# Kernel tuning notes

Hardware: AMD Instinct MI355X
Metric: run time of the kernel (lower is better)

The kernel has to match this reference:

```python
import jax, jax.numpy as jnp
import numpy as np

N, E, B, D, R, L = 60000, 600000, 512, 128, 30, 3
CUT_LOW, CUT_HIGH = 0.0, 10.0
N_ATOM_TYPES = 100


def _sp(x, beta, threshold):
    # torch.nn.Softplus(beta, threshold): x if beta*x > threshold else log1p(exp(beta*x))/beta
    bx = beta * x
    return jnp.where(bx > threshold, x, jnp.log1p(jnp.exp(jnp.minimum(bx, threshold))) / beta)


def setup_inputs() -> dict:
    key = jax.random.key(0)
    ks = jax.random.split(key, 16)

    def lin(k, fi, fo):
        k1, k2 = jax.random.split(k)
        W = jax.random.normal(k1, (fi, fo), jnp.float32) * (fi ** -0.5)
        b = jax.random.normal(k2, (fo,), jnp.float32) * 0.01
        return W, b

    def lin_stack(k, fi, fo, n):
        Ws, bs = zip(*[lin(kk, fi, fo) for kk in jax.random.split(k, n)])
        return jnp.stack(Ws), jnp.stack(bs)

    inp = {}
    inp['atom_type'] = jax.random.randint(ks[0], (N,), 0, N_ATOM_TYPES)
    inp['src'] = jax.random.randint(ks[1], (E,), 0, N)
    inp['dst'] = jax.random.randint(ks[2], (E,), 0, N)
    inp['graph_ids'] = jnp.sort(jax.random.randint(ks[3], (N,), 0, B))
    inp['dist'] = jax.random.uniform(ks[4], (E,), jnp.float32) * CUT_HIGH
    inp['node_emb'] = jax.random.normal(ks[5], (N_ATOM_TYPES, D), jnp.float32) * 0.1
    inp['W_n1'], inp['b_n1'] = lin_stack(ks[6], D, D, L)
    inp['W_c1'], inp['b_c1'] = lin_stack(ks[7], R, D, L)
    inp['W_c2'], inp['b_c2'] = lin_stack(ks[8], D, D, L)
    inp['W_c3'], inp['b_c3'] = lin_stack(ks[9], D, D, L)
    inp['W_n2'], inp['b_n2'] = lin_stack(ks[10], D, D, L)
    inp['W_n3'], inp['b_n3'] = lin_stack(ks[11], D, D, L)
    inp['W_r1'], inp['b_r1'] = lin(ks[12], D * (L + 1), 64)
    inp['W_r2'], inp['b_r2'] = lin(ks[13], 64, 1)
    return inp


def reference(atom_type, src, dst, graph_ids, dist, node_emb,
              W_n1, b_n1, W_c1, b_c1, W_c2, b_c2, W_c3, b_c3,
              W_n2, b_n2, W_n3, b_n3, W_r1, b_r1, W_r2, b_r2):
    # RBF expansion of edge distances: exp(-(d - mu_k)^2 / gap)  -> [E, R]
    centers = jnp.linspace(CUT_LOW, CUT_HIGH, R).astype(dist.dtype)
    gap = centers[1] - centers[0]
    rbf = jnp.exp(-((dist[:, None] - centers) ** 2) / gap)

    h = node_emb[atom_type]  # node embedding lookup [N, D]
    hs = [h]
    for i in range(L):  # MultiLevelInteraction layers (fixed small count)
        h_new = hs[-1] @ W_n1[i] + b_n1[i]                       # node_layer1 [N, D]
        # VEConv edge MLP on rbf (linear1 -> softplus(0.5,14) -> linear2 -> linear3)
        e = _sp(rbf @ W_c1[i] + b_c1[i], 0.5, 14.0) @ W_c2[i] + b_c2[i]
        e = e @ W_c3[i] + b_c3[i]                                 # [E, D]
        # sum_e(h_new[src]*e) + sum_e(e) fused into one scatter-sum over dst
        msg = (h_new[src] + 1.0) * e                              # [E, D]
        node = jax.ops.segment_sum(msg, dst, num_segments=N)      # [N, D]
        new_node = _sp(node @ W_n2[i] + b_n2[i], 0.5, 14.0) @ W_n3[i] + b_n3[i]
        hs.append(hs[-1] + new_node)                              # residual h_i
    hcat = jnp.concatenate(hs, axis=1)                            # [N, D*(L+1)]
    out = _sp(hcat @ W_r1 + b_r1, 1.0, 20.0) @ W_r2 + b_r2        # [N, 1]
    # dgl.sum_nodes per molecule, then flatten -> [B]
    return jax.ops.segment_sum(out[:, 0], graph_ids, num_segments=B)
```

## Files before the change

kernel.cpp:

```cpp
#include <hip/hip_runtime.h>
#include <math.h>

#define N_NODES 60000
#define N_EDGES 600000
#define B_GRAPHS 512
#define DIM 128
#define RBF_R 30
#define NLAYERS 3
#define NBINS 1024
#define CHUNK 512
#define NCHUNK ((N_NODES + CHUNK - 1) / CHUNK)

typedef __attribute__((ext_vector_type(8))) short bf16x8;
typedef __attribute__((ext_vector_type(4))) float f32x4;

__device__ __forceinline__ float sp05(float x) {
    float bx = 0.5f * x;
    return bx > 14.0f ? x : 2.0f * log1pf(expf(bx));
}
__device__ __forceinline__ float sp1(float x) {
    return x > 20.0f ? x : log1pf(expf(x));
}
__device__ __forceinline__ unsigned short f2bf(float f) {
    unsigned int u = __float_as_uint(f);
    unsigned int r = u + 0x7FFFu + ((u >> 16) & 1u);
    return (unsigned short)(r >> 16);
}
__device__ __forceinline__ float bf2f(unsigned int s) {
    return __uint_as_float(s << 16);
}


__global__ void k_convW(const float* __restrict__ Wn1, const float* __restrict__ Wn2,
                        const float* __restrict__ Wn3, unsigned short* __restrict__ WtF) {
    int i = blockIdx.x * 256 + threadIdx.x;
    int mat = i >> 14, r = i & 16383;
    int frag = r >> 9, within = r & 511;
    int ks = frag >> 3, ntile = frag & 7;
    int lane = within >> 3, j = within & 7;
    int q = lane >> 4, l16 = lane & 15;
    int n = ntile * 16 + l16;
    int k = ks * 32 + q * 8 + j;
    const float* src = (mat < 3) ? (Wn1 + (size_t)mat * 16384)
                     : (mat < 6) ? (Wn2 + (size_t)(mat - 3) * 16384)
                                 : (Wn3 + (size_t)(mat - 6) * 16384);
    WtF[i] = f2bf(src[k * 128 + n]);
}

__global__ void k_convR(const float* __restrict__ Wr1, unsigned short* __restrict__ Wr1tF) {
    int i = blockIdx.x * 256 + threadIdx.x;
    int frag = i >> 9, within = i & 511;
    int lvl = frag >> 4, ks = (frag >> 2) & 3, ntile = frag & 3;
    int lane = within >> 3, j = within & 7;
    int q = lane >> 4, l16 = lane & 15;
    int n = ntile * 16 + l16;
    int k = lvl * 128 + ks * 32 + q * 8 + j;
    Wr1tF[i] = f2bf(Wr1[k * 64 + n]);
}

__global__ void k_embed(const int* __restrict__ atom_type,
                        const float* __restrict__ node_emb,
                        float* __restrict__ h0, unsigned short* __restrict__ hb0) {
    int i = blockIdx.x * blockDim.x + threadIdx.x;
    if (i >= N_NODES * DIM) return;
    int n = i >> 7, d = i & 127;
    float v = node_emb[atom_type[n] * DIM + d];
    h0[i] = v;
    hb0[i] = f2bf(v);
}


__global__ void k_hist(const int* __restrict__ dst, int* __restrict__ counts) {
    int e = blockIdx.x * blockDim.x + threadIdx.x;
    if (e >= N_EDGES) return;
    atomicAdd(&counts[dst[e]], 1);
}

__global__ void k_bsum(const int* __restrict__ counts, int* __restrict__ bsums) {
    __shared__ int red[256];
    int c = blockIdx.x, tid = threadIdx.x;
    int base = c * CHUNK;
    int v = 0;
    for (int i = tid; i < CHUNK; i += 256)
        if (base + i < N_NODES) v += counts[base + i];
    red[tid] = v;
    __syncthreads();
    for (int s = 128; s > 0; s >>= 1) {
        if (tid < s) red[tid] += red[tid + s];
        __syncthreads();
    }
    if (tid == 0) bsums[c] = red[0];
}

__global__ void k_scan_b(int* __restrict__ bsums) {
    __shared__ int sb[NCHUNK];
    int tid = threadIdx.x;
    if (tid < NCHUNK) sb[tid] = bsums[tid];
    __syncthreads();
    if (tid == 0) {
        int run = 0;
        for (int i = 0; i < NCHUNK; ++i) { int v = sb[i]; sb[i] = run; run += v; }
    }
    __syncthreads();
    if (tid < NCHUNK) bsums[tid] = sb[tid];
}

__global__ void k_scan_final(const int* __restrict__ counts, const int* __restrict__ bsums,
                             int* __restrict__ offsets) {
    __shared__ int sc[CHUNK];
    int c = blockIdx.x, tid = threadIdx.x;
    int base = c * CHUNK;
    for (int i = tid; i < CHUNK; i += 256)
        sc[i] = (base + i < N_NODES) ? counts[base + i] : 0;
    __syncthreads();
    if (tid == 0) {
        int run = bsums[c];
        for (int i = 0; i < CHUNK; ++i) { int v = sc[i]; sc[i] = run; run += v; }
    }
    __syncthreads();
    for (int i = tid; i < CHUNK; i += 256)
        if (base + i < N_NODES) offsets[base + i] = sc[i];
    if (c == 0 && tid == 0) offsets[N_NODES] = N_EDGES;
}

__global__ void k_fill(const int* __restrict__ src, const int* __restrict__ dst,
                       const float* __restrict__ dist,
                       const int* __restrict__ offsets, int* __restrict__ cnt2,
                       int* __restrict__ srcp, int* __restrict__ binp,
                       float* __restrict__ wp) {
    int e = blockIdx.x * blockDim.x + threadIdx.x;
    if (e >= N_EDGES) return;
    int d = dst[e];
    int pos = offsets[d] + atomicAdd(&cnt2[d], 1);
    srcp[pos] = src[e];
    float x = dist[e];
    float p = x * ((float)NBINS / 10.0f);
    int bin = (int)p;
    if (bin > NBINS - 1) bin = NBINS - 1;
    binp[pos] = bin;
    wp[pos] = p - (float)bin;
}


__global__ void k_table(const float* __restrict__ Wc1, const float* __restrict__ bc1,
                        const float* __restrict__ Wc2, const float* __restrict__ bc2,
                        const float* __restrict__ Wc3, const float* __restrict__ bc3,
                        unsigned short* __restrict__ tableb) {
    __shared__ float t[DIM];
    __shared__ float u[DIM];
    int b = blockIdx.x;
    int d = threadIdx.x;
    float dist = (float)b * (10.0f / (float)NBINS);
    const float gap = 10.0f / 29.0f;
    float acc = bc1[d];
#pragma unroll
    for (int k = 0; k < RBF_R; ++k) {
        float c = (float)k * (10.0f / 29.0f);
        float df = dist - c;
        acc += expf(-df * df / gap) * Wc1[k * DIM + d];
    }
    t[d] = sp05(acc);
    __syncthreads();
    acc = bc2[d];
#pragma unroll 8
    for (int k = 0; k < DIM; ++k) acc += t[k] * Wc2[k * DIM + d];
    u[d] = acc;
    __syncthreads();
    acc = bc3[d];
#pragma unroll 8
    for (int k = 0; k < DIM; ++k) acc += u[k] * Wc3[k * DIM + d];
    tableb[b * DIM + d] = f2bf(acc);
}

__global__ void k_pack(const unsigned short* __restrict__ tableb,
                       unsigned int* __restrict__ packed) {
    int i = blockIdx.x * 256 + threadIdx.x;
    float a = bf2f(tableb[i]);
    float b = bf2f(tableb[i + DIM]);
    packed[i] = (unsigned int)f2bf(a) | ((unsigned int)f2bf(b - a) << 16);
}

__global__ __launch_bounds__(256) void k_gemm_g(const unsigned short* __restrict__ Ab,
                                                const unsigned short* __restrict__ WtF,
                                                const float* __restrict__ bias,
                                                unsigned short* __restrict__ Cb) {
    int tid = threadIdx.x;
    int wave = tid >> 6, lane = tid & 63;
    int q = lane >> 4, l16 = lane & 15;
    int mhalf = wave & 1, nhalf = wave >> 1;
    int rb = blockIdx.x * 64 + mhalf * 32;
    int c0 = nhalf * 64;
    bf16x8 bfrag[4][4];
#pragma unroll
    for (int ks = 0; ks < 4; ++ks)
#pragma unroll
        for (int nt = 0; nt < 4; ++nt)
            bfrag[ks][nt] = *(const bf16x8*)&WtF[(size_t)(ks * 8 + nhalf * 4 + nt) * 512 + lane * 8];
    f32x4 acc[2][4] = {};
#pragma unroll
    for (int ks = 0; ks < 4; ++ks)
#pragma unroll
        for (int mt = 0; mt < 2; ++mt) {
            int m = rb + mt * 16 + l16;
            if (m > N_NODES - 1) m = N_NODES - 1;
            bf16x8 a = *(const bf16x8*)&Ab[(size_t)m * 128 + ks * 32 + q * 8];
#pragma unroll
            for (int nt = 0; nt < 4; ++nt)
                acc[mt][nt] = __builtin_amdgcn_mfma_f32_16x16x32_bf16(a, bfrag[ks][nt], acc[mt][nt], 0, 0, 0);
        }
#pragma unroll
    for (int mt = 0; mt < 2; ++mt)
#pragma unroll
        for (int nt = 0; nt < 4; ++nt) {
            int col = c0 + nt * 16 + l16;
            float b = bias[col] + 1.0f;
#pragma unroll
            for (int r = 0; r < 4; ++r) {
                int row = rb + mt * 16 + q * 4 + r;
                if (row < N_NODES) Cb[(size_t)row * 128 + col] = f2bf(acc[mt][nt][r] + b);
            }
        }
}

__global__ __launch_bounds__(256) void k_gather(
    const int* __restrict__ offsets, const int* __restrict__ srcp,
    const int* __restrict__ binp, const float* __restrict__ wp,
    const unsigned int* __restrict__ packed, const unsigned short* __restrict__ gb,
    unsigned short* __restrict__ nodeb) {
    int wave = threadIdx.x >> 6, lane = threadIdx.x & 63;
    int n = blockIdx.x * 4 + wave;
    int beg = offsets[n], end = offsets[n + 1];
    float acc0 = 0.f, acc1 = 0.f, acc2 = 0.f, acc3 = 0.f;
    int j = beg;
    for (; j + 2 <= end; j += 2) {
        int s0 = srcp[j],   s1 = srcp[j + 1];
        int b0 = binp[j],   b1 = binp[j + 1];
        float w0 = wp[j],   w1 = wp[j + 1];
        uint2 p0 = *(const uint2*)&packed[(size_t)b0 * DIM + lane * 2];
        uint2 p1 = *(const uint2*)&packed[(size_t)b1 * DIM + lane * 2];
        unsigned int g0 = *(const unsigned int*)&gb[(size_t)s0 * DIM + lane * 2];
        unsigned int g1 = *(const unsigned int*)&gb[(size_t)s1 * DIM + lane * 2];
        acc0 += bf2f(g0 & 0xffff) * (bf2f(p0.x & 0xffff) + w0 * bf2f(p0.x >> 16));
        acc1 += bf2f(g0 >> 16)    * (bf2f(p0.y & 0xffff) + w0 * bf2f(p0.y >> 16));
        acc2 += bf2f(g1 & 0xffff) * (bf2f(p1.x & 0xffff) + w1 * bf2f(p1.x >> 16));
        acc3 += bf2f(g1 >> 16)    * (bf2f(p1.y & 0xffff) + w1 * bf2f(p1.y >> 16));
    }
    if (j < end) {
        int s0 = srcp[j];
        int b0 = binp[j];
        float w0 = wp[j];
        uint2 p0 = *(const uint2*)&packed[(size_t)b0 * DIM + lane * 2];
        unsigned int g0 = *(const unsigned int*)&gb[(size_t)s0 * DIM + lane * 2];
        acc0 += bf2f(g0 & 0xffff) * (bf2f(p0.x & 0xffff) + w0 * bf2f(p0.x >> 16));
        acc1 += bf2f(g0 >> 16)    * (bf2f(p0.y & 0xffff) + w0 * bf2f(p0.y >> 16));
    }
    acc0 += acc2; acc1 += acc3;
    unsigned int o = (unsigned int)f2bf(acc0) | ((unsigned int)f2bf(acc1) << 16);
    *(unsigned int*)&nodeb[(size_t)n * DIM + lane * 2] = o;
}

__global__ __launch_bounds__(256) void k_node_update(
    const unsigned short* __restrict__ nodeb,
    const unsigned short* __restrict__ W2tF, const float* __restrict__ b2,
    const unsigned short* __restrict__ W3tF, const float* __restrict__ b3,
    const float* __restrict__ h_in, float* __restrict__ h_out,
    unsigned short* __restrict__ hb_out) {
    __shared__ unsigned short ts[64][136];
    int tid = threadIdx.x;
    int wave = tid >> 6, lane = tid & 63;
    int q = lane >> 4, l16 = lane & 15;
    int mhalf = wave & 1, nhalf = wave >> 1;
    int rb = blockIdx.x * 64 + mhalf * 32;
    int c0 = nhalf * 64;

    bf16x8 bfrag[4][4];
#pragma unroll
    for (int ks = 0; ks < 4; ++ks)
#pragma unroll
        for (int nt = 0; nt < 4; ++nt)
            bfrag[ks][nt] = *(const bf16x8*)&W2tF[(size_t)(ks * 8 + nhalf * 4 + nt) * 512 + lane * 8];
    f32x4 acc[2][4] = {};
#pragma unroll
    for (int ks = 0; ks < 4; ++ks)
#pragma unroll
        for (int mt = 0; mt < 2; ++mt) {
            int m = rb + mt * 16 + l16;
            if (m > N_NODES - 1) m = N_NODES - 1;
            bf16x8 a = *(const bf16x8*)&nodeb[(size_t)m * 128 + ks * 32 + q * 8];
#pragma unroll
            for (int nt = 0; nt < 4; ++nt)
                acc[mt][nt] = __builtin_amdgcn_mfma_f32_16x16x32_bf16(a, bfrag[ks][nt], acc[mt][nt], 0, 0, 0);
        }
#pragma unroll
    for (int mt = 0; mt < 2; ++mt)
#pragma unroll
        for (int nt = 0; nt < 4; ++nt) {
            int col = c0 + nt * 16 + l16;
            float b = b2[col];
#pragma unroll
            for (int r = 0; r < 4; ++r) {
                int lrow = mhalf * 32 + mt * 16 + q * 4 + r;
                ts[lrow][col] = f2bf(sp05(acc[mt][nt][r] + b));
            }
        }
    __syncthreads();
#pragma unroll
    for (int ks = 0; ks < 4; ++ks)
#pragma unroll
        for (int nt = 0; nt < 4; ++nt)
            bfrag[ks][nt] = *(const bf16x8*)&W3tF[(size_t)(ks * 8 + nhalf * 4 + nt) * 512 + lane * 8];
#pragma unroll
    for (int mt = 0; mt < 2; ++mt)
#pragma unroll
        for (int nt = 0; nt < 4; ++nt) acc[mt][nt] = (f32x4){0.f, 0.f, 0.f, 0.f};
#pragma unroll
    for (int ks = 0; ks < 4; ++ks)
#pragma unroll
        for (int mt = 0; mt < 2; ++mt) {
            int lrow = mhalf * 32 + mt * 16 + l16;
            bf16x8 a = *(const bf16x8*)&ts[lrow][ks * 32 + q * 8];
#pragma unroll
            for (int nt = 0; nt < 4; ++nt)
                acc[mt][nt] = __builtin_amdgcn_mfma_f32_16x16x32_bf16(a, bfrag[ks][nt], acc[mt][nt], 0, 0, 0);
        }
#pragma unroll
    for (int mt = 0; mt < 2; ++mt)
#pragma unroll
        for (int nt = 0; nt < 4; ++nt) {
            int col = c0 + nt * 16 + l16;
            float b = b3[col];
#pragma unroll
            for (int r = 0; r < 4; ++r) {
                int row = rb + mt * 16 + q * 4 + r;
                if (row < N_NODES) {
                    size_t idx = (size_t)row * 128 + col;
                    float v = h_in[idx] + acc[mt][nt][r] + b;
                    h_out[idx] = v;
                    hb_out[idx] = f2bf(v);
                }
            }
        }
}

__global__ __launch_bounds__(256) void k_readout(
    const unsigned short* __restrict__ hb0, const unsigned short* __restrict__ hb1,
    const unsigned short* __restrict__ hb2, const unsigned short* __restrict__ hb3,
    const unsigned short* __restrict__ Wr1tF, const float* __restrict__ br1,
    const float* __restrict__ Wr2, const float* __restrict__ br2,
    const int* __restrict__ graph_ids, float* __restrict__ out) {
    int tid = threadIdx.x;
    int wave = tid >> 6, lane = tid & 63;
    int q = lane >> 4, l16 = lane & 15;
    int rb = blockIdx.x * 64 + wave * 16;
    const unsigned short* hbs[4] = {hb0, hb1, hb2, hb3};
    f32x4 acc[4] = {};
    for (int lvl = 0; lvl < 4; ++lvl) {
        bf16x8 bfrag[4][4];
#pragma unroll
        for (int ks = 0; ks < 4; ++ks)
#pragma unroll
            for (int nt = 0; nt < 4; ++nt)
                bfrag[ks][nt] = *(const bf16x8*)&Wr1tF[(size_t)((lvl * 4 + ks) * 4 + nt) * 512 + lane * 8];
        const unsigned short* Ab = hbs[lvl];
#pragma unroll
        for (int ks = 0; ks < 4; ++ks) {
            int m = rb + l16;
            if (m > N_NODES - 1) m = N_NODES - 1;
            bf16x8 a = *(const bf16x8*)&Ab[(size_t)m * 128 + ks * 32 + q * 8];
#pragma unroll
            for (int nt = 0; nt < 4; ++nt)
                acc[nt] = __builtin_amdgcn_mfma_f32_16x16x32_bf16(a, bfrag[ks][nt], acc[nt], 0, 0, 0);
        }
    }
    float brr = br2[0];
    float partial[4] = {0.f, 0.f, 0.f, 0.f};
#pragma unroll
    for (int nt = 0; nt < 4; ++nt) {
        int col = nt * 16 + l16;
        float b = br1[col];
        float w = Wr2[col];
#pragma unroll
        for (int r = 0; r < 4; ++r) partial[r] += sp1(acc[nt][r] + b) * w;
    }
#pragma unroll
    for (int r = 0; r < 4; ++r) {
        float v = partial[r];
        v += __shfl_xor(v, 1); v += __shfl_xor(v, 2);
        v += __shfl_xor(v, 4); v += __shfl_xor(v, 8);
        if (l16 == 0) {
            int row = rb + q * 4 + r;
            if (row < N_NODES) atomicAdd(&out[graph_ids[row]], v + brr);
        }
    }
}

extern "C" void kernel_launch(void* const* d_in, const int* in_sizes, int n_in,
                              void* d_out, int out_size, void* d_ws, size_t ws_size,
                              hipStream_t stream) {
    const int* atom_type   = (const int*)d_in[0];
    const int* src         = (const int*)d_in[1];
    const int* dst         = (const int*)d_in[2];
    const int* graph_ids   = (const int*)d_in[3];
    const float* dist      = (const float*)d_in[4];
    const float* node_emb  = (const float*)d_in[5];
    const float* W_n1 = (const float*)d_in[6];  const float* b_n1 = (const float*)d_in[7];
    const float* W_c1 = (const float*)d_in[8];  const float* b_c1 = (const float*)d_in[9];
    const float* W_c2 = (const float*)d_in[10]; const float* b_c2 = (const float*)d_in[11];
    const float* W_c3 = (const float*)d_in[12]; const float* b_c3 = (const float*)d_in[13];
    const float* W_n2 = (const float*)d_in[14]; const float* b_n2 = (const float*)d_in[15];
    const float* W_n3 = (const float*)d_in[16]; const float* b_n3 = (const float*)d_in[17];
    const float* W_r1 = (const float*)d_in[18]; const float* b_r1 = (const float*)d_in[19];
    const float* W_r2 = (const float*)d_in[20]; const float* b_r2 = (const float*)d_in[21];
    float* out = (float*)d_out;

    size_t ND = (size_t)N_NODES * DIM;
    float* h_even = (float*)d_ws;
    float* h_odd  = h_even + ND;
    float* wp     = h_odd + ND;
    int* offsets  = (int*)(wp + N_EDGES);
    int* srcp     = offsets + 60008;
    int* binp     = srcp + N_EDGES;
    int* counts   = binp + N_EDGES;
    int* cnt2     = counts + N_NODES;
    int* bsums    = cnt2 + N_NODES;
    unsigned int* packed = (unsigned int*)(bsums + 128);
    unsigned short* hb0    = (unsigned short*)(packed + (size_t)NBINS * DIM);
    unsigned short* hb1    = hb0 + ND;
    unsigned short* hb2    = hb1 + ND;
    unsigned short* hb3    = hb2 + ND;
    unsigned short* gb     = hb3 + ND;
    unsigned short* nodeb  = gb + ND;
    unsigned short* tableb = nodeb + ND;
    unsigned short* WtF    = tableb + (size_t)(NBINS + 1) * DIM;
    unsigned short* Wr1tF  = WtF + 9 * 16384;

    unsigned short* hbp[4] = {hb0, hb1, hb2, hb3};
    float* hcur = h_even;
    float* hnext = h_odd;

    hipMemsetAsync(out, 0, B_GRAPHS * sizeof(float), stream);
    hipMemsetAsync(counts, 0, (2 * N_NODES + 128) * sizeof(int), stream);

    k_convW<<<(9 * 16384) / 256, 256, 0, stream>>>(W_n1, W_n2, W_n3, WtF);
    k_convR<<<32768 / 256, 256, 0, stream>>>(W_r1, Wr1tF);
    k_embed<<<(N_NODES * DIM) / 256, 256, 0, stream>>>(atom_type, node_emb, h_even, hb0);

    k_hist<<<(N_EDGES + 255) / 256, 256, 0, stream>>>(dst, counts);
    k_bsum<<<NCHUNK, 256, 0, stream>>>(counts, bsums);
    k_scan_b<<<1, 128, 0, stream>>>(bsums);
    k_scan_final<<<NCHUNK, 256, 0, stream>>>(counts, bsums, offsets);
    k_fill<<<(N_EDGES + 255) / 256, 256, 0, stream>>>(src, dst, dist, offsets, cnt2,
                                                      srcp, binp, wp);

    int gblocks = (N_NODES + 63) / 64;
    for (int i = 0; i < NLAYERS; ++i) {
        k_table<<<NBINS + 1, DIM, 0, stream>>>(
            W_c1 + (size_t)i * RBF_R * DIM, b_c1 + (size_t)i * DIM,
            W_c2 + (size_t)i * DIM * DIM,  b_c2 + (size_t)i * DIM,
            W_c3 + (size_t)i * DIM * DIM,  b_c3 + (size_t)i * DIM, tableb);
        k_pack<<<(NBINS * DIM) / 256, 256, 0, stream>>>(tableb, packed);
        k_gemm_g<<<gblocks, 256, 0, stream>>>(
            hbp[i], WtF + (size_t)i * 16384, b_n1 + (size_t)i * DIM, gb);
        k_gather<<<N_NODES / 4, 256, 0, stream>>>(offsets, srcp, binp, wp, packed, gb, nodeb);
        k_node_update<<<gblocks, 256, 0, stream>>>(
            nodeb, WtF + (size_t)(3 + i) * 16384, b_n2 + (size_t)i * DIM,
            WtF + (size_t)(6 + i) * 16384, b_n3 + (size_t)i * DIM,
            hcur, hnext, hbp[i + 1]);
        float* tmp = hcur; hcur = hnext; hnext = tmp;
    }
    k_readout<<<gblocks, 256, 0, stream>>>(
        hb0, hb1, hb2, hb3, Wr1tF, b_r1, W_r2, b_r2, graph_ids, out);
}
```

Baseline: 669.8 us.

## Pack edge metadata into uint2, unroll gather by four, restructure readout tiling

Edge source, bin index and quantized interpolation weight are packed into one 8-byte record per edge, so the gather kernel does one load instead of three separate array loads. The gather loop is unrolled to four edges per iteration to keep more independent memory requests in flight. The readout kernel stages the full W_r1 fragment set in shared memory and processes 128 rows per block with two M tiles, reusing the B fragments across both. The interpolation weight is now quantized to 16 bits, which adds a small precision loss, and the readout uses 64KB of LDS per block, which may reduce occupancy.

```diff
diff --git a/kernel.cpp b/kernel.cpp
--- a/kernel.cpp
+++ b/kernel.cpp
@@ -126,19 +126,19 @@
 __global__ void k_fill(const int* __restrict__ src, const int* __restrict__ dst,
                        const float* __restrict__ dist,
                        const int* __restrict__ offsets, int* __restrict__ cnt2,
-                       int* __restrict__ srcp, int* __restrict__ binp,
-                       float* __restrict__ wp) {
+                       uint2* __restrict__ meta) {
     int e = blockIdx.x * blockDim.x + threadIdx.x;
     if (e >= N_EDGES) return;
     int d = dst[e];
     int pos = offsets[d] + atomicAdd(&cnt2[d], 1);
-    srcp[pos] = src[e];
     float x = dist[e];
     float p = x * ((float)NBINS / 10.0f);
     int bin = (int)p;
     if (bin > NBINS - 1) bin = NBINS - 1;
-    binp[pos] = bin;
-    wp[pos] = p - (float)bin;
+    float w = p - (float)bin;
+    int wq = (int)(w * 65535.0f + 0.5f);
+    if (wq > 65535) wq = 65535;
+    meta[pos] = make_uint2((unsigned)src[e], ((unsigned)bin << 16) | (unsigned)wq);
 }
 
 
@@ -223,40 +223,50 @@
 }
 
 __global__ __launch_bounds__(256) void k_gather(
-    const int* __restrict__ offsets, const int* __restrict__ srcp,
-    const int* __restrict__ binp, const float* __restrict__ wp,
+    const int* __restrict__ offsets, const uint2* __restrict__ meta,
     const unsigned int* __restrict__ packed, const unsigned short* __restrict__ gb,
     unsigned short* __restrict__ nodeb) {
     int wave = threadIdx.x >> 6, lane = threadIdx.x & 63;
     int n = blockIdx.x * 4 + wave;
     int beg = offsets[n], end = offsets[n + 1];
+    int off = lane * 2;
+    const float ws = 1.0f / 65535.0f;
     float acc0 = 0.f, acc1 = 0.f, acc2 = 0.f, acc3 = 0.f;
     int j = beg;
-    for (; j + 2 <= end; j += 2) {
-        int s0 = srcp[j],   s1 = srcp[j + 1];
-        int b0 = binp[j],   b1 = binp[j + 1];
-        float w0 = wp[j],   w1 = wp[j + 1];
-        uint2 p0 = *(const uint2*)&packed[(size_t)b0 * DIM + lane * 2];
-        uint2 p1 = *(const uint2*)&packed[(size_t)b1 * DIM + lane * 2];
-        unsigned int g0 = *(const unsigned int*)&gb[(size_t)s0 * DIM + lane * 2];
-        unsigned int g1 = *(const unsigned int*)&gb[(size_t)s1 * DIM + lane * 2];
+    for (; j + 4 <= end; j += 4) {
+        uint2 m0 = meta[j], m1 = meta[j + 1], m2 = meta[j + 2], m3 = meta[j + 3];
+        uint2 p0 = *(const uint2*)&packed[(size_t)(m0.y >> 16) * DIM + off];
+        uint2 p1 = *(const uint2*)&packed[(size_t)(m1.y >> 16) * DIM + off];
+        uint2 p2 = *(const uint2*)&packed[(size_t)(m2.y >> 16) * DIM + off];
+        uint2 p3 = *(const uint2*)&packed[(size_t)(m3.y >> 16) * DIM + off];
+        unsigned int g0 = *(const unsigned int*)&gb[(size_t)m0.x * DIM + off];
+        unsigned int g1 = *(const unsigned int*)&gb[(size_t)m1.x * DIM + off];
+        unsigned int g2 = *(const unsigned int*)&gb[(size_t)m2.x * DIM + off];
+        unsigned int g3 = *(const unsigned int*)&gb[(size_t)m3.x * DIM + off];
+        float w0 = (float)(m0.y & 0xffff) * ws;
+        float w1 = (float)(m1.y & 0xffff) * ws;
+        float w2 = (float)(m2.y & 0xffff) * ws;
+        float w3 = (float)(m3.y & 0xffff) * ws;
         acc0 += bf2f(g0 & 0xffff) * (bf2f(p0.x & 0xffff) + w0 * bf2f(p0.x >> 16));
         acc1 += bf2f(g0 >> 16)    * (bf2f(p0.y & 0xffff) + w0 * bf2f(p0.y >> 16));
         acc2 += bf2f(g1 & 0xffff) * (bf2f(p1.x & 0xffff) + w1 * bf2f(p1.x >> 16));
         acc3 += bf2f(g1 >> 16)    * (bf2f(p1.y & 0xffff) + w1 * bf2f(p1.y >> 16));
-    }
-    if (j < end) {
-        int s0 = srcp[j];
-        int b0 = binp[j];
-        float w0 = wp[j];
-        uint2 p0 = *(const uint2*)&packed[(size_t)b0 * DIM + lane * 2];
-        unsigned int g0 = *(const unsigned int*)&gb[(size_t)s0 * DIM + lane * 2];
+        acc0 += bf2f(g2 & 0xffff) * (bf2f(p2.x & 0xffff) + w2 * bf2f(p2.x >> 16));
+        acc1 += bf2f(g2 >> 16)    * (bf2f(p2.y & 0xffff) + w2 * bf2f(p2.y >> 16));
+        acc2 += bf2f(g3 & 0xffff) * (bf2f(p3.x & 0xffff) + w3 * bf2f(p3.x >> 16));
+        acc3 += bf2f(g3 >> 16)    * (bf2f(p3.y & 0xffff) + w3 * bf2f(p3.y >> 16));
+    }
+    for (; j < end; ++j) {
+        uint2 m0 = meta[j];
+        uint2 p0 = *(const uint2*)&packed[(size_t)(m0.y >> 16) * DIM + off];
+        unsigned int g0 = *(const unsigned int*)&gb[(size_t)m0.x * DIM + off];
+        float w0 = (float)(m0.y & 0xffff) * ws;
         acc0 += bf2f(g0 & 0xffff) * (bf2f(p0.x & 0xffff) + w0 * bf2f(p0.x >> 16));
         acc1 += bf2f(g0 >> 16)    * (bf2f(p0.y & 0xffff) + w0 * bf2f(p0.y >> 16));
     }
     acc0 += acc2; acc1 += acc3;
     unsigned int o = (unsigned int)f2bf(acc0) | ((unsigned int)f2bf(acc1) << 16);
-    *(unsigned int*)&nodeb[(size_t)n * DIM + lane * 2] = o;
+    *(unsigned int*)&nodeb[(size_t)n * DIM + off] = o;
 }
 
 __global__ __launch_bounds__(256) void k_node_update(
@@ -348,48 +358,63 @@
     const unsigned short* __restrict__ Wr1tF, const float* __restrict__ br1,
     const float* __restrict__ Wr2, const float* __restrict__ br2,
     const int* __restrict__ graph_ids, float* __restrict__ out) {
+    __shared__ uint4 sB4[4096];
     int tid = threadIdx.x;
+    const uint4* wsrc = (const uint4*)Wr1tF;
+    for (int i = tid; i < 4096; i += 256) sB4[i] = wsrc[i];
+    __syncthreads();
+    const unsigned short* sB = (const unsigned short*)sB4;
     int wave = tid >> 6, lane = tid & 63;
     int q = lane >> 4, l16 = lane & 15;
-    int rb = blockIdx.x * 64 + wave * 16;
+    int rb0 = blockIdx.x * 128 + wave * 16;
     const unsigned short* hbs[4] = {hb0, hb1, hb2, hb3};
-    f32x4 acc[4] = {};
+    f32x4 acc[2][4] = {};
     for (int lvl = 0; lvl < 4; ++lvl) {
-        bf16x8 bfrag[4][4];
+        bf16x8 bf[4][4];
 #pragma unroll
         for (int ks = 0; ks < 4; ++ks)
 #pragma unroll
             for (int nt = 0; nt < 4; ++nt)
-                bfrag[ks][nt] = *(const bf16x8*)&Wr1tF[(size_t)((lvl * 4 + ks) * 4 + nt) * 512 + lane * 8];
+                bf[ks][nt] = *(const bf16x8*)&sB[(size_t)((lvl * 4 + ks) * 4 + nt) * 512 + lane * 8];
         const unsigned short* Ab = hbs[lvl];
-#pragma unroll
-        for (int ks = 0; ks < 4; ++ks) {
-            int m = rb + l16;
-            if (m > N_NODES - 1) m = N_NODES - 1;
-            bf16x8 a = *(const bf16x8*)&Ab[(size_t)m * 128 + ks * 32 + q * 8];
-#pragma unroll
-            for (int nt = 0; nt < 4; ++nt)
-                acc[nt] = __builtin_amdgcn_mfma_f32_16x16x32_bf16(a, bfrag[ks][nt], acc[nt], 0, 0, 0);
-        }
+        bf16x8 a[2][4];
+#pragma unroll
+        for (int mt = 0; mt < 2; ++mt)
+#pragma unroll
+            for (int ks = 0; ks < 4; ++ks) {
+                int m = rb0 + mt * 64 + l16;
+                if (m > N_NODES - 1) m = N_NODES - 1;
+                a[mt][ks] = *(const bf16x8*)&Ab[(size_t)m * 128 + ks * 32 + q * 8];
+            }
+#pragma unroll
+        for (int ks = 0; ks < 4; ++ks)
+#pragma unroll
+            for (int mt = 0; mt < 2; ++mt)
+#pragma unroll
+                for (int nt = 0; nt < 4; ++nt)
+                    acc[mt][nt] = __builtin_amdgcn_mfma_f32_16x16x32_bf16(a[mt][ks], bf[ks][nt], acc[mt][nt], 0, 0, 0);
     }
     float brr = br2[0];
-    float partial[4] = {0.f, 0.f, 0.f, 0.f};
-#pragma unroll
-    for (int nt = 0; nt < 4; ++nt) {
-        int col = nt * 16 + l16;
-        float b = br1[col];
-        float w = Wr2[col];
-#pragma unroll
-        for (int r = 0; r < 4; ++r) partial[r] += sp1(acc[nt][r] + b) * w;
-    }
-#pragma unroll
-    for (int r = 0; r < 4; ++r) {
-        float v = partial[r];
-        v += __shfl_xor(v, 1); v += __shfl_xor(v, 2);
-        v += __shfl_xor(v, 4); v += __shfl_xor(v, 8);
-        if (l16 == 0) {
-            int row = rb + q * 4 + r;
-            if (row < N_NODES) atomicAdd(&out[graph_ids[row]], v + brr);
+#pragma unroll
+    for (int mt = 0; mt < 2; ++mt) {
+        float partial[4] = {0.f, 0.f, 0.f, 0.f};
+#pragma unroll
+        for (int nt = 0; nt < 4; ++nt) {
+            int col = nt * 16 + l16;
+            float b = br1[col];
+            float w = Wr2[col];
+#pragma unroll
+            for (int r = 0; r < 4; ++r) partial[r] += sp1(acc[mt][nt][r] + b) * w;
+        }
+#pragma unroll
+        for (int r = 0; r < 4; ++r) {
+            float v = partial[r];
+            v += __shfl_xor(v, 1); v += __shfl_xor(v, 2);
+            v += __shfl_xor(v, 4); v += __shfl_xor(v, 8);
+            if (l16 == 0) {
+                int row = rb0 + mt * 64 + q * 4 + r;
+                if (row < N_NODES) atomicAdd(&out[graph_ids[row]], v + brr);
+            }
         }
     }
 }
@@ -416,11 +441,9 @@
     size_t ND = (size_t)N_NODES * DIM;
     float* h_even = (float*)d_ws;
     float* h_odd  = h_even + ND;
-    float* wp     = h_odd + ND;
-    int* offsets  = (int*)(wp + N_EDGES);
-    int* srcp     = offsets + 60008;
-    int* binp     = srcp + N_EDGES;
-    int* counts   = binp + N_EDGES;
+    uint2* meta   = (uint2*)(h_odd + ND);
+    int* offsets  = (int*)(meta + N_EDGES);
+    int* counts   = offsets + 60008;
     int* cnt2     = counts + N_NODES;
     int* bsums    = cnt2 + N_NODES;
     unsigned int* packed = (unsigned int*)(bsums + 128);
@@ -449,10 +472,10 @@
     k_bsum<<<NCHUNK, 256, 0, stream>>>(counts, bsums);
     k_scan_b<<<1, 128, 0, stream>>>(bsums);
     k_scan_final<<<NCHUNK, 256, 0, stream>>>(counts, bsums, offsets);
-    k_fill<<<(N_EDGES + 255) / 256, 256, 0, stream>>>(src, dst, dist, offsets, cnt2,
-                                                      srcp, binp, wp);
+    k_fill<<<(N_EDGES + 255) / 256, 256, 0, stream>>>(src, dst, dist, offsets, cnt2, meta);
 
     int gblocks = (N_NODES + 63) / 64;
+    int rblocks = (N_NODES + 127) / 128;
     for (int i = 0; i < NLAYERS; ++i) {
         k_table<<<NBINS + 1, DIM, 0, stream>>>(
             W_c1 + (size_t)i * RBF_R * DIM, b_c1 + (size_t)i * DIM,
@@ -461,13 +484,13 @@
         k_pack<<<(NBINS * DIM) / 256, 256, 0, stream>>>(tableb, packed);
         k_gemm_g<<<gblocks, 256, 0, stream>>>(
             hbp[i], WtF + (size_t)i * 16384, b_n1 + (size_t)i * DIM, gb);
-        k_gather<<<N_NODES / 4, 256, 0, stream>>>(offsets, srcp, binp, wp, packed, gb, nodeb);
+        k_gather<<<N_NODES / 4, 256, 0, stream>>>(offsets, meta, packed, gb, nodeb);
         k_node_update<<<gblocks, 256, 0, stream>>>(
             nodeb, WtF + (size_t)(3 + i) * 16384, b_n2 + (size_t)i * DIM,
             WtF + (size_t)(6 + i) * 16384, b_n3 + (size_t)i * DIM,
             hcur, hnext, hbp[i + 1]);
         float* tmp = hcur; hcur = hnext; hnext = tmp;
     }
-    k_readout<<<gblocks, 256, 0, stream>>>(
+    k_readout<<<rblocks, 256, 0, stream>>>(
         hb0, hb1, hb2, hb3, Wr1tF, b_r1, W_r2, b_r2, graph_ids, out);
 }
```

Measured after the change: 640.7 us. -4.3%, faster.
